# Kernel optimization log

Hardware: AMD Instinct MI355X
Metric: run time of the kernel (lower is better)

## Reference

```python
import jax, jax.numpy as jnp
import numpy as np

S, B, V, D, H, G = 60, 256, 50000, 300, 512, 15  # seq, batch, vocab, embed/proj, hidden, grid
DM, DOUT = 1024, 2
MLP_IN = G * G + 7  # 225 pooled + 7 extra features = 232


def setup_inputs() -> dict:
    key = jax.random.key(0)
    ks = jax.random.split(key, 16)
    n = lambda k, shp: (jax.random.normal(k, shp, jnp.float32) * 0.02)
    return {
        "embed_table": n(ks[0], (V, D)),
        "proj_W": n(ks[1], (D, D)),
        "proj_b": jnp.zeros((D,), jnp.float32),
        "bn_g": jnp.ones((D,), jnp.float32),
        "bn_b": jnp.zeros((D,), jnp.float32),
        "Wih": n(ks[2], (4 * H, D)),
        "Whh": n(ks[3], (4 * H, H)),
        "bih": jnp.zeros((4 * H,), jnp.float32),
        "bhh": jnp.zeros((4 * H,), jnp.float32),
        "W1": n(ks[4], (DM, MLP_IN)),
        "b1": jnp.zeros((DM,), jnp.float32),
        "g1": jnp.ones((DM,), jnp.float32),
        "be1": jnp.zeros((DM,), jnp.float32),
        "W2": n(ks[5], (DM, DM)),
        "b2": jnp.zeros((DM,), jnp.float32),
        "g2": jnp.ones((DM,), jnp.float32),
        "be2": jnp.zeros((DM,), jnp.float32),
        "W3": n(ks[6], (DOUT, DM)),
        "b3": jnp.zeros((DOUT,), jnp.float32),
        "extra_feats": jax.random.normal(ks[7], (B, 7), jnp.float32),
        "sentence1": jax.random.randint(ks[8], (S, B), 0, V, jnp.int32),
        "sentence2": jax.random.randint(ks[9], (S, B), 0, V, jnp.int32),
    }


def _bn(x, g, b, axes):
    mu = x.mean(axis=axes, keepdims=True)
    var = x.var(axis=axes, keepdims=True)
    return (x - mu) * jax.lax.rsqrt(var + 1e-5) * g + b


def reference(embed_table, proj_W, proj_b, bn_g, bn_b, Wih, Whh, bih, bhh,
              W1, b1, g1, be1, W2, b2, g2, be2, W3, b3,
              extra_feats, sentence1, sentence2):
    def encode(tokens):
        e = embed_table[tokens]                      # [S,B,D] gather
        e = e @ proj_W.T + proj_b                    # Bottle Linear over S*B rows
        e = _bn(e, bn_g, bn_b, (0, 1))               # Bottle BatchNorm over S*B rows

        def step(carry, x):
            h, c = carry
            z = x @ Wih.T + h @ Whh.T + (bih + bhh)  # [B,4H], gate order i,f,g,o
            i, f, g_, o = jnp.split(z, 4, axis=-1)
            c = jax.nn.sigmoid(f) * c + jax.nn.sigmoid(i) * jnp.tanh(g_)
            h = jax.nn.sigmoid(o) * jnp.tanh(c)
            return (h, c), h

        init = (jnp.zeros((B, H), e.dtype), jnp.zeros((B, H), e.dtype))
        _, hs = jax.lax.scan(step, init, e)          # [S,B,H]
        return hs.transpose(1, 0, 2)                 # [B,S,H]

    h1 = encode(sentence1)
    h2 = encode(sentence2)

    # pairwise L2 distance matrix per batch element: [B,S,S]
    sq = (jnp.sum(h1 * h1, -1)[:, :, None]
          + jnp.sum(h2 * h2, -1)[:, None, :]
          - 2.0 * jnp.einsum('bid,bjd->bij', h1, h2))
    dist = jnp.sqrt(jnp.maximum(sq, 0.0) + 1e-12)

    # dynamic 15x15 min-pool (S divisible by G => kernel = S//G)
    k = S // G
    pooled = dist.reshape(B, G, k, G, k).min(axis=(2, 4)).reshape(B, G * G)

    x = jnp.concatenate([pooled, extra_feats], axis=1)  # [B,232]
    x = _bn(jax.nn.relu(x @ W1.T + b1), g1, be1, (0,))
    x = _bn(jax.nn.relu(x @ W2.T + b2), g2, be2, (0,))
    return jax.nn.log_softmax(x @ W3.T + b3, axis=-1)   # [B,2]
```

## Files before the change

kernel.cpp:

```cpp
#include <hip/hip_runtime.h>
#include <hip/hip_bf16.h>

#define S_LEN 60
#define BATCH 256
#define EMB   300
#define EMBP  320
#define HID   512
#define DMLP  1024
#define NROW  (2*S_LEN*BATCH)
#define RPS   (S_LEN*BATCH)

typedef __attribute__((ext_vector_type(8))) short short8v;
typedef __attribute__((ext_vector_type(4))) float f32x4;

static __device__ __forceinline__ float sigf(float x){
  return 1.0f/(1.0f+__expf(-x));
}
static __device__ __forceinline__ float tanh_fast(float x){
  x = fminf(fmaxf(x,-40.0f),40.0f);
  float a = __expf(2.0f*x);
  return (a-1.0f)/(a+1.0f);
}
static __device__ __forceinline__ unsigned short f2b(float v){
  __hip_bfloat16 h = __float2bfloat16(v);
  return *(unsigned short*)&h;
}
static __device__ __forceinline__ float b2f(unsigned short u){
  return __uint_as_float(((unsigned int)u)<<16);
}

__global__ __launch_bounds__(256) void k_conv_weights(
    const float* __restrict__ Wih, const float* __restrict__ Whh,
    const float* __restrict__ bih, const float* __restrict__ bhh,
    const float* __restrict__ projW,
    unsigned short* __restrict__ Wihb, unsigned short* __restrict__ Whhb,
    unsigned short* __restrict__ projWb, float* __restrict__ bsum)
{
  const int tid = blockIdx.x*256 + threadIdx.x;
  const int stride = gridDim.x*256;
  for (int i=tid; i<2048*EMBP; i+=stride){
    int n = i/EMBP, k = i - n*EMBP;
    Wihb[i] = f2b((k<EMB) ? Wih[(size_t)n*EMB + k] : 0.0f);
  }
  for (int i=tid; i<2048*HID; i+=stride) Whhb[i] = f2b(Whh[i]);
  for (int i=tid; i<EMBP*EMBP; i+=stride){
    int n = i/EMBP, k = i - n*EMBP;
    projWb[i] = f2b((n<EMB && k<EMB) ? projW[(size_t)n*EMB + k] : 0.0f);
  }
  for (int i=tid; i<2048; i+=stride) bsum[i] = bih[i]+bhh[i];
}

__global__ __launch_bounds__(512) void k_embed_mfma(
    const float* __restrict__ embed, const unsigned short* __restrict__ projWb,
    const float* __restrict__ projb, const int* __restrict__ s1,
    const int* __restrict__ s2, unsigned short* __restrict__ Pb)
{
  __shared__ __align__(16) unsigned short sA0[64*40];
  __shared__ __align__(16) unsigned short sA1[64*40];
  __shared__ __align__(16) unsigned short sW0[64*40];
  __shared__ __align__(16) unsigned short sW1[64*40];
  __shared__ int stok[64];
  const int m0 = blockIdx.x*64, n0 = blockIdx.y*64;
  const int tid = threadIdx.x;
  if (tid < 64){
    int r = m0 + tid;
    stok[tid] = (r < RPS) ? s1[r] : s2[r-RPS];
  }
  __syncthreads();
  const int lane = tid & 63, w = tid>>6;
  const int wr = w>>2, wc = w&3;
  const bool isA = tid < 256;
  const int srow = (tid&255)>>2, sseg = tid&3;
  const float* Arow = embed + (size_t)stok[srow]*EMB;
  const unsigned short* Wrow = projWb + (size_t)(n0+srow)*EMBP;

  const int ldst = srow*40 + sseg*8;
  const int aoff0 = (wr*32 + (lane&15))*40 + (lane>>4)*8;
  const int aoff1 = aoff0 + 16*40;
  const int woff  = (wc*16 + (lane&15))*40 + (lane>>4)*8;

  f32x4 acc0 = {0.f,0.f,0.f,0.f}, acc1 = {0.f,0.f,0.f,0.f};

  auto loadA = [&](int kk)->uint4 {
    int kb = kk*32 + sseg*8;
    unsigned short t8[8];
    if (kb+7 < EMB){
      float4 f0 = *(const float4*)(Arow + kb);
      float4 f1 = *(const float4*)(Arow + kb + 4);
      t8[0]=f2b(f0.x); t8[1]=f2b(f0.y); t8[2]=f2b(f0.z); t8[3]=f2b(f0.w);
      t8[4]=f2b(f1.x); t8[5]=f2b(f1.y); t8[6]=f2b(f1.z); t8[7]=f2b(f1.w);
    } else {
      #pragma unroll
      for (int jq=0; jq<8; jq++){
        int k = kb+jq;
        t8[jq] = f2b((k<EMB) ? Arow[k] : 0.0f);
      }
    }
    uint4 o;
    o.x = (unsigned)t8[0] | ((unsigned)t8[1]<<16);
    o.y = (unsigned)t8[2] | ((unsigned)t8[3]<<16);
    o.z = (unsigned)t8[4] | ((unsigned)t8[5]<<16);
    o.w = (unsigned)t8[6] | ((unsigned)t8[7]<<16);
    return o;
  };

  if (isA) *(uint4*)(sA0 + ldst) = loadA(0);
  else     *(uint4*)(sW0 + ldst) = *(const uint4*)(Wrow + sseg*8);
  __syncthreads();

  for (int kk=0; kk<10; kk++){
    uint4 nv;
    if (kk < 9){
      if (isA) nv = loadA(kk+1);
      else     nv = *(const uint4*)(Wrow + (kk+1)*32 + sseg*8);
    }
    const unsigned short* A = (kk&1) ? sA1 : sA0;
    const unsigned short* W = (kk&1) ? sW1 : sW0;
    short8v af0 = *(const short8v*)(A + aoff0);
    short8v af1 = *(const short8v*)(A + aoff1);
    short8v wf  = *(const short8v*)(W + woff);
    acc0 = __builtin_amdgcn_mfma_f32_16x16x32_bf16(af0, wf, acc0, 0,0,0);
    acc1 = __builtin_amdgcn_mfma_f32_16x16x32_bf16(af1, wf, acc1, 0,0,0);
    if (kk < 9){
      unsigned short* dst = ((kk&1) ? (isA?sA0:sW0) : (isA?sA1:sW1)) + ldst;
      *(uint4*)dst = nv;
    }
    __syncthreads();
  }

  const int cc = wc*16 + (lane&15);
  const int n = n0 + cc;
  const float bias = (n < EMB) ? projb[n] : 0.0f;
  const bool valid = (n < EMB);
  #pragma unroll
  for (int v=0; v<4; v++){
    int r0 = wr*32 + (lane>>4)*4 + v;
    Pb[(size_t)(m0+r0)*EMBP + n]    = f2b(valid ? acc0[v]+bias : 0.0f);
    Pb[(size_t)(m0+r0+16)*EMBP + n] = f2b(valid ? acc1[v]+bias : 0.0f);
  }
}

__global__ __launch_bounds__(320) void k_bn_partial(const unsigned short* __restrict__ Pb,
    float* __restrict__ ps, float* __restrict__ psq)
{
  const int rb = blockIdx.x, sent = blockIdx.y, t = threadIdx.x;
  if (t >= EMB) return;
  const unsigned short* base = Pb + ((size_t)sent*RPS + (size_t)rb*256)*EMBP;
  float s=0.0f, q=0.0f;
  for (int r=0;r<256;r++){
    float v = b2f(base[(size_t)r*EMBP + t]);
    s += v; q = fmaf(v,v,q);
  }
  ps [(size_t)(sent*60+rb)*EMB + t] = s;
  psq[(size_t)(sent*60+rb)*EMB + t] = q;
}

__global__ __launch_bounds__(320) void k_bn_final(const float* __restrict__ ps,
    const float* __restrict__ psq, const float* __restrict__ g,
    const float* __restrict__ b, float* __restrict__ scale, float* __restrict__ shift)
{
  const int sent = blockIdx.x, t = threadIdx.x;
  if (t >= EMB) return;
  float s=0.0f, q=0.0f;
  for (int i=0;i<60;i++){
    s += ps [(size_t)(sent*60+i)*EMB + t];
    q += psq[(size_t)(sent*60+i)*EMB + t];
  }
  float mean = s * (1.0f/15360.0f);
  float var  = q * (1.0f/15360.0f) - mean*mean;
  float sc = g[t] * rsqrtf(var + 1e-5f);
  scale[sent*EMB+t] = sc;
  shift[sent*EMB+t] = b[t] - mean*sc;
}

__global__ __launch_bounds__(256) void k_bn_apply(unsigned short* __restrict__ Pb,
    const float* __restrict__ scale, const float* __restrict__ shift)
{
  const int r = blockIdx.x*8 + (threadIdx.x>>5);
  const int c0 = threadIdx.x & 31;
  const int sent = (r >= RPS) ? 1 : 0;
  unsigned short* row = Pb + (size_t)r*EMBP;
  for (int c=c0; c<EMB; c+=32){
    float v = b2f(row[c]);
    v = fmaf(v, scale[sent*EMB+c], shift[sent*EMB+c]);
    row[c] = f2b(v);
  }
}

__global__ __launch_bounds__(512) void k_lstm_step(
    const unsigned short* __restrict__ Pb,
    const unsigned short* __restrict__ Wihb,
    const unsigned short* __restrict__ Whhb,
    const float* __restrict__ bsum,
    const unsigned short* __restrict__ Hin,
    unsigned short* __restrict__ Hnext,
    float* __restrict__ cst,
    unsigned short* __restrict__ Hout,
    int tstep)
{
  __shared__ __align__(16) unsigned short smem[4*5120];
  float* zs = (float*)smem;

  const int tid = threadIdx.x;
  const int lane = tid & 63, w = tid >> 6;
  const int wr = w >> 2, wc = w & 3;
  const int j0 = (int)blockIdx.x * 16;
  const int m0 = (int)blockIdx.y * 64;
  const int sent = m0 >> 8;
  const int brow = m0 & 255;

  const int half = tid >> 8;
  const int rs = tid & 255;
  const int srow = rs >> 2, sseg = rs & 3;
  const int kb = half*32 + sseg*8;
  const int ldst = half*2560 + srow*40 + sseg*8;

  const unsigned short* pAx = Pb + ((size_t)((sent*S_LEN + tstep)*BATCH) + brow + srow)*EMBP + kb;
  const unsigned short* pAh = Hin + (size_t)(m0 + srow)*HID + kb;
  const int wn = (srow>>4)*HID + j0 + (srow&15);
  const unsigned short* pWx = Wihb + (size_t)wn*EMBP + kb;
  const unsigned short* pWh = Whhb + (size_t)wn*HID  + kb;

  auto loadA = [&](int c)->uint4 {
    return (c < 5) ? *(const uint4*)(pAx + c*64) : *(const uint4*)(pAh + (c-5)*64);
  };
  auto loadW = [&](int c)->uint4 {
    return (c < 5) ? *(const uint4*)(pWx + c*64) : *(const uint4*)(pWh + (c-5)*64);
  };

  const int aoffB = (wr*32 + (lane&15))*40 + (lane>>4)*8;
  const int woffB = (wc*16 + (lane&15))*40 + (lane>>4)*8;

  f32x4 acc0 = {0.f,0.f,0.f,0.f}, acc1 = {0.f,0.f,0.f,0.f};

  uint4 rA[3], rW[3];
  rA[0] = loadA(0); rW[0] = loadW(0);
  rA[1] = loadA(1); rW[1] = loadW(1);
  rA[2] = loadA(2); rW[2] = loadW(2);
  *(uint4*)(smem + ldst)         = rA[0];
  *(uint4*)(smem + 10240 + ldst) = rW[0];
  __syncthreads();

  #pragma unroll
  for (int kk = 0; kk < 13; kk++){
    if (kk + 3 < 13){
      rA[(kk+3)%3] = loadA(kk+3);
      rW[(kk+3)%3] = loadW(kk+3);
    }
    const unsigned short* A = smem + (kk&1)*5120;
    const unsigned short* W = smem + 10240 + (kk&1)*5120;
    #pragma unroll
    for (int h2 = 0; h2 < 2; h2++){
      const int bh = h2*2560;
      short8v wf = *(const short8v*)(W + bh + woffB);
      short8v a0 = *(const short8v*)(A + bh + aoffB);
      short8v a1 = *(const short8v*)(A + bh + aoffB + 16*40);
      acc0 = __builtin_amdgcn_mfma_f32_16x16x32_bf16(a0, wf, acc0, 0,0,0);
      acc1 = __builtin_amdgcn_mfma_f32_16x16x32_bf16(a1, wf, acc1, 0,0,0);
    }
    if (kk + 1 < 13){
      *(uint4*)(smem + ((kk+1)&1)*5120 + ldst)         = rA[(kk+1)%3];
      *(uint4*)(smem + 10240 + ((kk+1)&1)*5120 + ldst) = rW[(kk+1)%3];
    }
    __syncthreads();
  }

  #pragma unroll
  for (int v = 0; v < 4; v++){
    int r0 = wr*32 + (lane>>4)*4 + v;
    int cc = wc*16 + (lane&15);
    zs[r0*66 + cc]      = acc0[v];
    zs[(r0+16)*66 + cc] = acc1[v];
  }
  __syncthreads();

  const int row_e = tid >> 4, jj = tid & 15, j = j0 + jj;
  const float zb0 = bsum[0*HID+j], zb1 = bsum[1*HID+j];
  const float zb2 = bsum[2*HID+j], zb3 = bsum[3*HID+j];
  #pragma unroll
  for (int q = 0; q < 2; q++){
    int row = row_e + q*32;
    int r = m0 + row;
    float zi = zs[row*66 + jj]    + zb0;
    float zf = zs[row*66 + 16+jj] + zb1;
    float zg = zs[row*66 + 32+jj] + zb2;
    float zo = zs[row*66 + 48+jj] + zb3;
    size_t ci = (size_t)r*HID + j;
    float cn = fmaf(sigf(zf), cst[ci], sigf(zi)*tanh_fast(zg));
    cst[ci] = cn;
    float hn = sigf(zo)*tanh_fast(cn);
    unsigned short hb = f2b(hn);
    Hnext[ci] = hb;
    Hout[((size_t)((sent*S_LEN + tstep)*BATCH) + (r&255))*HID + j] = hb;
  }
}

#define SDU 258
__global__ __launch_bounds__(256) void k_dist_pool(
    const unsigned short* __restrict__ Hout, float* __restrict__ pooled)
{
  __shared__ unsigned int h1s[S_LEN*SDU];
  __shared__ unsigned int h2s[S_LEN*SDU];
  __shared__ float n1s[S_LEN], n2s[S_LEN];
  const int b = blockIdx.x, tid = threadIdx.x;
  const unsigned int* H = (const unsigned int*)Hout;
  for (int e=tid; e<S_LEN*256; e+=256){
    int row = e>>8, cu = e&255;
    h1s[row*SDU+cu] = H[((size_t)(0*S_LEN+row)*BATCH + b)*256 + cu];
    h2s[row*SDU+cu] = H[((size_t)(1*S_LEN+row)*BATCH + b)*256 + cu];
  }
  __syncthreads();
  if (tid < S_LEN){
    const unsigned int* rp = &h1s[tid*SDU];
    float q=0.0f;
    for (int cu=0;cu<256;cu++){
      unsigned int u = rp[cu];
      float lo = __uint_as_float(u<<16);
      float hi = __uint_as_float(u & 0xffff0000u);
      q = fmaf(lo,lo,q); q = fmaf(hi,hi,q);
    }
    n1s[tid] = q;
  } else if (tid >= 64 && tid < 64+S_LEN){
    const unsigned int* rp = &h2s[(tid-64)*SDU];
    float q=0.0f;
    for (int cu=0;cu<256;cu++){
      unsigned int u = rp[cu];
      float lo = __uint_as_float(u<<16);
      float hi = __uint_as_float(u & 0xffff0000u);
      q = fmaf(lo,lo,q); q = fmaf(hi,hi,q);
    }
    n2s[tid-64] = q;
  }
  __syncthreads();
  if (tid < 225){
    const int gi = tid/15, gj = tid%15;
    float acc[4][4];
    #pragma unroll
    for (int a=0;a<4;a++)
      #pragma unroll
      for (int c=0;c<4;c++) acc[a][c]=0.0f;
    const unsigned int* r1[4]; const unsigned int* r2[4];
    #pragma unroll
    for (int a=0;a<4;a++){ r1[a]=&h1s[(gi*4+a)*SDU]; r2[a]=&h2s[(gj*4+a)*SDU]; }
    for (int cu=0;cu<256;cu++){
      float lo1[4],hi1[4],lo2[4],hi2[4];
      #pragma unroll
      for (int a=0;a<4;a++){
        unsigned int u = r1[a][cu];
        lo1[a]=__uint_as_float(u<<16); hi1[a]=__uint_as_float(u&0xffff0000u);
      }
      #pragma unroll
      for (int c=0;c<4;c++){
        unsigned int u = r2[c][cu];
        lo2[c]=__uint_as_float(u<<16); hi2[c]=__uint_as_float(u&0xffff0000u);
      }
      #pragma unroll
      for (int a=0;a<4;a++)
        #pragma unroll
        for (int c=0;c<4;c++)
          acc[a][c] = fmaf(lo1[a],lo2[c], fmaf(hi1[a],hi2[c], acc[a][c]));
    }
    float mn = 3.4e38f;
    #pragma unroll
    for (int a=0;a<4;a++)
      #pragma unroll
      for (int c=0;c<4;c++){
        float sq = n1s[gi*4+a] + n2s[gj*4+c] - 2.0f*acc[a][c];
        mn = fminf(mn, sqrtf(fmaxf(sq,0.0f)+1e-12f));
      }
    pooled[(size_t)b*225 + tid] = mn;
  }
}

__global__ __launch_bounds__(256) void k_mlp1(const float* __restrict__ pooled,
    const float* __restrict__ extra, const float* __restrict__ W1,
    const float* __restrict__ b1, float* __restrict__ y1)
{
  __shared__ __align__(16) float xs[232];
  const int b = blockIdx.x, tid = threadIdx.x;
  if (tid < 225) xs[tid] = pooled[(size_t)b*225 + tid];
  else if (tid < 232) xs[tid] = extra[(size_t)b*7 + (tid-225)];
  __syncthreads();
  #pragma unroll
  for (int q=0;q<4;q++){
    int n = tid + q*256;
    float acc = b1[n];
    const float4* wr = (const float4*)(W1 + (size_t)n*232);
    const float4* xr = (const float4*)xs;
    for (int k4=0;k4<58;k4++){
      float4 w = wr[k4]; float4 x = xr[k4];
      acc = fmaf(w.x,x.x, fmaf(w.y,x.y, fmaf(w.z,x.z, fmaf(w.w,x.w, acc))));
    }
    y1[(size_t)b*DMLP + n] = fmaxf(acc, 0.0f);
  }
}

__global__ __launch_bounds__(256) void k_mlp_bn2(const float* __restrict__ y,
    const float* __restrict__ g, const float* __restrict__ be,
    float* __restrict__ scale, float* __restrict__ shift)
{
  __shared__ float sred[256], qred[256];
  const int c0 = blockIdx.x*64;
  const int ch = threadIdx.x & 63, grp = threadIdx.x >> 6;
  const int n = c0 + ch;
  float s=0.0f, q=0.0f;
  for (int b=grp*64; b<grp*64+64; b++){
    float v = y[(size_t)b*DMLP + n];
    s += v; q = fmaf(v,v,q);
  }
  sred[threadIdx.x]=s; qred[threadIdx.x]=q;
  __syncthreads();
  if (grp==0){
    s = sred[ch] + sred[64+ch] + sred[128+ch] + sred[192+ch];
    q = qred[ch] + qred[64+ch] + qred[128+ch] + qred[192+ch];
    float mean = s * (1.0f/256.0f);
    float var  = q * (1.0f/256.0f) - mean*mean;
    float sc = g[n] * rsqrtf(var + 1e-5f);
    scale[n] = sc;
    shift[n] = be[n] - mean*sc;
  }
}

__global__ __launch_bounds__(256) void k_mlp2_gemm(
    const float* __restrict__ y1, const float* __restrict__ scale1,
    const float* __restrict__ shift1, const float* __restrict__ W2,
    float* __restrict__ y2part)
{
  __shared__ float As[64][33];
  __shared__ float Bs[64][33];
  const int n0 = blockIdx.x*64, m0 = blockIdx.y*64;
  const int kbase = blockIdx.z*256;
  const int tid = threadIdx.x;
  const int tx = tid & 15, ty = tid >> 4;
  float acc[4][4];
  #pragma unroll
  for (int a=0;a<4;a++)
    #pragma unroll
    for (int b=0;b<4;b++) acc[a][b]=0.0f;

  for (int k0=0; k0<256; k0+=32){
    #pragma unroll
    for (int i=0;i<8;i++){
      int e = tid + i*256;
      int rl = e>>5, kl = e&31;
      int kk = kbase + k0 + kl;
      As[rl][kl] = fmaf(y1[(size_t)(m0+rl)*DMLP + kk], scale1[kk], shift1[kk]);
      Bs[rl][kl] = W2[(size_t)(n0+rl)*DMLP + kk];
    }
    __syncthreads();
    #pragma unroll
    for (int kk=0;kk<32;kk++){
      float a[4], w[4];
      #pragma unroll
      for (int rl=0;rl<4;rl++) a[rl] = As[ty*4+rl][kk];
      #pragma unroll
      for (int cj=0;cj<4;cj++) w[cj] = Bs[cj*16+tx][kk];
      #pragma unroll
      for (int rl=0;rl<4;rl++)
        #pragma unroll
        for (int cj=0;cj<4;cj++) acc[rl][cj] = fmaf(a[rl], w[cj], acc[rl][cj]);
    }
    __syncthreads();
  }
  float* dst = y2part + ((size_t)blockIdx.z*BATCH)*DMLP;
  #pragma unroll
  for (int rl=0;rl<4;rl++){
    int r = m0 + ty*4 + rl;
    #pragma unroll
    for (int cj=0;cj<4;cj++){
      int n = n0 + cj*16 + tx;
      dst[(size_t)r*DMLP + n] = acc[rl][cj];
    }
  }
}

__global__ __launch_bounds__(256) void k_mlp2_fin(
    const float* __restrict__ y2part, const float* __restrict__ b2,
    float* __restrict__ y2)
{
  const int b = blockIdx.x;
  const int n = threadIdx.x*4;
  float4 p0 = *(const float4*)(y2part + ((size_t)(0*BATCH + b))*DMLP + n);
  float4 p1 = *(const float4*)(y2part + ((size_t)(1*BATCH + b))*DMLP + n);
  float4 p2 = *(const float4*)(y2part + ((size_t)(2*BATCH + b))*DMLP + n);
  float4 p3 = *(const float4*)(y2part + ((size_t)(3*BATCH + b))*DMLP + n);
  float4 bb = *(const float4*)(b2 + n);
  float4 o;
  o.x = fmaxf(p0.x+p1.x+p2.x+p3.x+bb.x, 0.0f);
  o.y = fmaxf(p0.y+p1.y+p2.y+p3.y+bb.y, 0.0f);
  o.z = fmaxf(p0.z+p1.z+p2.z+p3.z+bb.z, 0.0f);
  o.w = fmaxf(p0.w+p1.w+p2.w+p3.w+bb.w, 0.0f);
  *(float4*)(y2 + (size_t)b*DMLP + n) = o;
}

__global__ __launch_bounds__(256) void k_mlp3(const float* __restrict__ y2,
    const float* __restrict__ scale2, const float* __restrict__ shift2,
    const float* __restrict__ W3, const float* __restrict__ b3,
    float* __restrict__ out)
{
  __shared__ float r0[256], r1[256];
  const int b = blockIdx.x, tid = threadIdx.x;
  float p0=0.0f, p1=0.0f;
  #pragma unroll
  for (int q=0;q<4;q++){
    int k = tid + q*256;
    float x = fmaf(y2[(size_t)b*DMLP + k], scale2[k], shift2[k]);
    p0 = fmaf(x, W3[k], p0);
    p1 = fmaf(x, W3[DMLP+k], p1);
  }
  r0[tid]=p0; r1[tid]=p1;
  __syncthreads();
  for (int s=128; s>0; s>>=1){
    if (tid<s){ r0[tid]+=r0[tid+s]; r1[tid]+=r1[tid+s]; }
    __syncthreads();
  }
  if (tid==0){
    float l0 = r0[0]+b3[0], l1 = r1[0]+b3[1];
    float m = fmaxf(l0,l1);
    float lse = m + logf(__expf(l0-m)+__expf(l1-m));
    out[b*2+0] = l0-lse;
    out[b*2+1] = l1-lse;
  }
}

extern "C" void kernel_launch(void* const* d_in, const int* in_sizes, int n_in,
                              void* d_out, int out_size, void* d_ws, size_t ws_size,
                              hipStream_t stream)
{
  (void)in_sizes; (void)n_in; (void)out_size; (void)ws_size;
  const float* embed = (const float*)d_in[0];
  const float* projW = (const float*)d_in[1];
  const float* projb = (const float*)d_in[2];
  const float* bn_g  = (const float*)d_in[3];
  const float* bn_b  = (const float*)d_in[4];
  const float* Wih   = (const float*)d_in[5];
  const float* Whh   = (const float*)d_in[6];
  const float* bih   = (const float*)d_in[7];
  const float* bhh   = (const float*)d_in[8];
  const float* W1    = (const float*)d_in[9];
  const float* b1    = (const float*)d_in[10];
  const float* g1    = (const float*)d_in[11];
  const float* be1   = (const float*)d_in[12];
  const float* W2    = (const float*)d_in[13];
  const float* b2    = (const float*)d_in[14];
  const float* g2    = (const float*)d_in[15];
  const float* be2   = (const float*)d_in[16];
  const float* W3    = (const float*)d_in[17];
  const float* b3    = (const float*)d_in[18];
  const float* extra = (const float*)d_in[19];
  const int*   s1    = (const int*)d_in[20];
  const int*   s2    = (const int*)d_in[21];
  float* out = (float*)d_out;

  float* ws = (float*)d_ws;
  size_t off = 0;
  float* ps   = ws + off; off += (size_t)2*60*EMB;
  float* psq  = ws + off; off += (size_t)2*60*EMB;
  float* bnsc = ws + off; off += 2*EMB;
  float* bnsh = ws + off; off += 2*EMB;
  float* bsum = ws + off; off += 2048;
  unsigned short* Pb     = (unsigned short*)(ws + off); off += (size_t)NROW*EMBP/2;
  unsigned short* Wihb   = (unsigned short*)(ws + off); off += (size_t)2048*EMBP/2;
  unsigned short* Whhb   = (unsigned short*)(ws + off); off += (size_t)2048*HID/2;
  unsigned short* projWb = (unsigned short*)(ws + off); off += (size_t)EMBP*EMBP/2;
  float* cst = ws + off; off += (size_t)512*HID;
  unsigned short* Hb0 = (unsigned short*)(ws + off); off += (size_t)512*HID/2;
  unsigned short* Hb1 = (unsigned short*)(ws + off); off += (size_t)512*HID/2;
  unsigned short* Hout = (unsigned short*)(ws + off); off += (size_t)2*S_LEN*BATCH*HID/2;
  float* pooled = ws + off; off += (size_t)BATCH*225;
  float* y1     = ws + off; off += (size_t)BATCH*DMLP;
  float* y2     = ws + off; off += (size_t)BATCH*DMLP;
  float* y2part = ws + off; off += (size_t)4*BATCH*DMLP;
  float* sc1    = ws + off; off += DMLP;
  float* sh1    = ws + off; off += DMLP;
  float* sc2    = ws + off; off += DMLP;
  float* sh2    = ws + off; off += DMLP;

  hipMemsetAsync(cst, 0, (size_t)(512*HID)*sizeof(float) + (size_t)(512*HID)*sizeof(unsigned short), stream);

  k_conv_weights<<<512, 256, 0, stream>>>(Wih, Whh, bih, bhh, projW,
                                          Wihb, Whhb, projWb, bsum);
  k_embed_mfma<<<dim3(NROW/64, 5), 512, 0, stream>>>(embed, projWb, projb, s1, s2, Pb);
  k_bn_partial<<<dim3(60,2), 320, 0, stream>>>(Pb, ps, psq);
  k_bn_final<<<2, 320, 0, stream>>>(ps, psq, bn_g, bn_b, bnsc, bnsh);
  k_bn_apply<<<NROW/8, 256, 0, stream>>>(Pb, bnsc, bnsh);

  for (int t=0; t<S_LEN; t++){
    const unsigned short* hin = (t & 1) ? Hb1 : Hb0;
    unsigned short*      hnxt = (t & 1) ? Hb0 : Hb1;
    k_lstm_step<<<dim3(32,8), 512, 0, stream>>>(Pb, Wihb, Whhb, bsum,
                                                hin, hnxt, cst, Hout, t);
  }

  k_dist_pool<<<BATCH, 256, 0, stream>>>(Hout, pooled);
  k_mlp1<<<BATCH, 256, 0, stream>>>(pooled, extra, W1, b1, y1);
  k_mlp_bn2<<<16, 256, 0, stream>>>(y1, g1, be1, sc1, sh1);
  k_mlp2_gemm<<<dim3(16,4,4), 256, 0, stream>>>(y1, sc1, sh1, W2, y2part);
  k_mlp2_fin<<<BATCH, 256, 0, stream>>>(y2part, b2, y2);
  k_mlp_bn2<<<16, 256, 0, stream>>>(y2, g2, be2, sc2, sh2);
  k_mlp3<<<BATCH, 256, 0, stream>>>(y2, sc2, sh2, W3, b3, out);
}
```

Before: 879.0 us.

## Widen LSTM step K-tile to 128 and tile the first MLP layer as a GEMM

The per-timestep LSTM kernel now stages 128 K columns per shared-memory stage instead of 64. This halves the number of barrier-separated iterations (7 instead of 13) at the cost of twice the LDS footprint. Separately, the first MLP layer moves from one block per batch row, which re-read all of W1 for every row, to a 64x64 register-tiled SIMT GEMM over a 16x4 grid. That GEMM reuses W1 and activations through shared memory, but runs far fewer blocks. The LSTM loop dominates the runtime because it is launched 60 times, so the fewer syncs per step are the main intended saving.

```diff
diff --git a/kernel.cpp b/kernel.cpp
--- a/kernel.cpp
+++ b/kernel.cpp
@@ -198,7 +198,7 @@
     unsigned short* __restrict__ Hout,
     int tstep)
 {
-  __shared__ __align__(16) unsigned short smem[4*5120];
+  __shared__ __align__(16) unsigned short smem[40960];
   float* zs = (float*)smem;
 
   const int tid = threadIdx.x;
@@ -209,23 +209,27 @@
   const int sent = m0 >> 8;
   const int brow = m0 & 255;
 
-  const int half = tid >> 8;
+  const int s0 = tid >> 8;
   const int rs = tid & 255;
   const int srow = rs >> 2, sseg = rs & 3;
-  const int kb = half*32 + sseg*8;
-  const int ldst = half*2560 + srow*40 + sseg*8;
-
-  const unsigned short* pAx = Pb + ((size_t)((sent*S_LEN + tstep)*BATCH) + brow + srow)*EMBP + kb;
-  const unsigned short* pAh = Hin + (size_t)(m0 + srow)*HID + kb;
+  const int kb0 = s0*32 + sseg*8;
+  const int kb1 = kb0 + 64;
+  const int ld0 = s0*2560 + srow*40 + sseg*8;
+  const int ld1 = ld0 + 5120;
+
+  const unsigned short* ArowP = Pb + ((size_t)((sent*S_LEN + tstep)*BATCH) + brow + srow)*EMBP;
+  const unsigned short* ArowH = Hin + (size_t)(m0 + srow)*HID;
   const int wn = (srow>>4)*HID + j0 + (srow&15);
-  const unsigned short* pWx = Wihb + (size_t)wn*EMBP + kb;
-  const unsigned short* pWh = Whhb + (size_t)wn*HID  + kb;
-
-  auto loadA = [&](int c)->uint4 {
-    return (c < 5) ? *(const uint4*)(pAx + c*64) : *(const uint4*)(pAh + (c-5)*64);
+  const unsigned short* WrowX = Wihb + (size_t)wn*EMBP;
+  const unsigned short* WrowH = Whhb + (size_t)wn*HID;
+
+  auto loadAc = [&](int col)->uint4 {
+    return (col < EMBP) ? *(const uint4*)(ArowP + col)
+                        : *(const uint4*)(ArowH + col - EMBP);
   };
-  auto loadW = [&](int c)->uint4 {
-    return (c < 5) ? *(const uint4*)(pWx + c*64) : *(const uint4*)(pWh + (c-5)*64);
+  auto loadWc = [&](int col)->uint4 {
+    return (col < EMBP) ? *(const uint4*)(WrowX + col)
+                        : *(const uint4*)(WrowH + col - EMBP);
   };
 
   const int aoffB = (wr*32 + (lane&15))*40 + (lane>>4)*8;
@@ -233,34 +237,50 @@
 
   f32x4 acc0 = {0.f,0.f,0.f,0.f}, acc1 = {0.f,0.f,0.f,0.f};
 
-  uint4 rA[3], rW[3];
-  rA[0] = loadA(0); rW[0] = loadW(0);
-  rA[1] = loadA(1); rW[1] = loadW(1);
-  rA[2] = loadA(2); rW[2] = loadW(2);
-  *(uint4*)(smem + ldst)         = rA[0];
-  *(uint4*)(smem + 10240 + ldst) = rW[0];
-  __syncthreads();
-
-  #pragma unroll
-  for (int kk = 0; kk < 13; kk++){
-    if (kk + 3 < 13){
-      rA[(kk+3)%3] = loadA(kk+3);
-      rW[(kk+3)%3] = loadW(kk+3);
-    }
-    const unsigned short* A = smem + (kk&1)*5120;
-    const unsigned short* W = smem + 10240 + (kk&1)*5120;
-    #pragma unroll
-    for (int h2 = 0; h2 < 2; h2++){
-      const int bh = h2*2560;
-      short8v wf = *(const short8v*)(W + bh + woffB);
-      short8v a0 = *(const short8v*)(A + bh + aoffB);
-      short8v a1 = *(const short8v*)(A + bh + aoffB + 16*40);
-      acc0 = __builtin_amdgcn_mfma_f32_16x16x32_bf16(a0, wf, acc0, 0,0,0);
-      acc1 = __builtin_amdgcn_mfma_f32_16x16x32_bf16(a1, wf, acc1, 0,0,0);
-    }
-    if (kk + 1 < 13){
-      *(uint4*)(smem + ((kk+1)&1)*5120 + ldst)         = rA[(kk+1)%3];
-      *(uint4*)(smem + 10240 + ((kk+1)&1)*5120 + ldst) = rW[(kk+1)%3];
+  {
+    uint4 a0 = loadAc(kb0), a1 = loadAc(kb1);
+    uint4 w0 = loadWc(kb0), w1 = loadWc(kb1);
+    *(uint4*)(smem + ld0) = a0;
+    *(uint4*)(smem + ld1) = a1;
+    *(uint4*)(smem + 20480 + ld0) = w0;
+    *(uint4*)(smem + 20480 + ld1) = w1;
+  }
+  __syncthreads();
+
+  #pragma unroll
+  for (int kk = 0; kk < 7; kk++){
+    uint4 pA0, pA1, pW0, pW1;
+    if (kk < 6){
+      int cbase = (kk+1)*128;
+      pA0 = loadAc(cbase + kb0);
+      pW0 = loadWc(cbase + kb0);
+      if (kk+1 < 6){
+        pA1 = loadAc(cbase + kb1);
+        pW1 = loadWc(cbase + kb1);
+      }
+    }
+    const unsigned short* A = smem + (kk&1)*10240;
+    const unsigned short* W = smem + 20480 + (kk&1)*10240;
+    #pragma unroll
+    for (int s = 0; s < 4; s++){
+      if (!(kk == 6 && s >= 2)){
+        const int bh = s*2560;
+        short8v wf  = *(const short8v*)(W + bh + woffB);
+        short8v a0f = *(const short8v*)(A + bh + aoffB);
+        short8v a1f = *(const short8v*)(A + bh + aoffB + 16*40);
+        acc0 = __builtin_amdgcn_mfma_f32_16x16x32_bf16(a0f, wf, acc0, 0,0,0);
+        acc1 = __builtin_amdgcn_mfma_f32_16x16x32_bf16(a1f, wf, acc1, 0,0,0);
+      }
+    }
+    if (kk < 6){
+      unsigned short* dA = smem + ((kk+1)&1)*10240;
+      unsigned short* dW = smem + 20480 + ((kk+1)&1)*10240;
+      *(uint4*)(dA + ld0) = pA0;
+      *(uint4*)(dW + ld0) = pW0;
+      if (kk+1 < 6){
+        *(uint4*)(dA + ld1) = pA1;
+        *(uint4*)(dW + ld1) = pW1;
+      }
     }
     __syncthreads();
   }
@@ -372,26 +392,58 @@
   }
 }
 
-__global__ __launch_bounds__(256) void k_mlp1(const float* __restrict__ pooled,
-    const float* __restrict__ extra, const float* __restrict__ W1,
-    const float* __restrict__ b1, float* __restrict__ y1)
-{
-  __shared__ __align__(16) float xs[232];
-  const int b = blockIdx.x, tid = threadIdx.x;
-  if (tid < 225) xs[tid] = pooled[(size_t)b*225 + tid];
-  else if (tid < 232) xs[tid] = extra[(size_t)b*7 + (tid-225)];
-  __syncthreads();
-  #pragma unroll
-  for (int q=0;q<4;q++){
-    int n = tid + q*256;
-    float acc = b1[n];
-    const float4* wr = (const float4*)(W1 + (size_t)n*232);
-    const float4* xr = (const float4*)xs;
-    for (int k4=0;k4<58;k4++){
-      float4 w = wr[k4]; float4 x = xr[k4];
-      acc = fmaf(w.x,x.x, fmaf(w.y,x.y, fmaf(w.z,x.z, fmaf(w.w,x.w, acc))));
-    }
-    y1[(size_t)b*DMLP + n] = fmaxf(acc, 0.0f);
+__global__ __launch_bounds__(256) void k_mlp1_gemm(
+    const float* __restrict__ pooled, const float* __restrict__ extra,
+    const float* __restrict__ W1, const float* __restrict__ b1,
+    float* __restrict__ y1)
+{
+  __shared__ float As[64][33];
+  __shared__ float Bs[64][33];
+  const int n0 = blockIdx.x*64, m0 = blockIdx.y*64;
+  const int tid = threadIdx.x;
+  const int tx = tid & 15, ty = tid >> 4;
+  float acc[4][4];
+  #pragma unroll
+  for (int a=0;a<4;a++)
+    #pragma unroll
+    for (int b=0;b<4;b++) acc[a][b]=0.0f;
+
+  for (int k0=0; k0<256; k0+=32){
+    #pragma unroll
+    for (int i=0;i<8;i++){
+      int e = tid + i*256;
+      int rl = e>>5, kl = e&31;
+      int c = k0 + kl;
+      float av;
+      if (c < 225)      av = pooled[(size_t)(m0+rl)*225 + c];
+      else if (c < 232) av = extra[(size_t)(m0+rl)*7 + (c-225)];
+      else              av = 0.0f;
+      As[rl][kl] = av;
+      Bs[rl][kl] = (c < 232) ? W1[(size_t)(n0+rl)*232 + c] : 0.0f;
+    }
+    __syncthreads();
+    #pragma unroll
+    for (int kk=0;kk<32;kk++){
+      float a[4], wv[4];
+      #pragma unroll
+      for (int rl=0;rl<4;rl++) a[rl] = As[ty*4+rl][kk];
+      #pragma unroll
+      for (int cj=0;cj<4;cj++) wv[cj] = Bs[cj*16+tx][kk];
+      #pragma unroll
+      for (int rl=0;rl<4;rl++)
+        #pragma unroll
+        for (int cj=0;cj<4;cj++) acc[rl][cj] = fmaf(a[rl], wv[cj], acc[rl][cj]);
+    }
+    __syncthreads();
+  }
+  #pragma unroll
+  for (int rl=0;rl<4;rl++){
+    int r = m0 + ty*4 + rl;
+    #pragma unroll
+    for (int cj=0;cj<4;cj++){
+      int n = n0 + cj*16 + tx;
+      y1[(size_t)r*DMLP + n] = fmaxf(acc[rl][cj] + b1[n], 0.0f);
+    }
   }
 }
 
@@ -593,7 +645,7 @@
   }
 
   k_dist_pool<<<BATCH, 256, 0, stream>>>(Hout, pooled);
-  k_mlp1<<<BATCH, 256, 0, stream>>>(pooled, extra, W1, b1, y1);
+  k_mlp1_gemm<<<dim3(16,4), 256, 0, stream>>>(pooled, extra, W1, b1, y1);
   k_mlp_bn2<<<16, 256, 0, stream>>>(y1, g1, be1, sc1, sh1);
   k_mlp2_gemm<<<dim3(16,4,4), 256, 0, stream>>>(y1, sc1, sh1, W2, y2part);
   k_mlp2_fin<<<BATCH, 256, 0, stream>>>(y2part, b2, y2);
```

Result: slower. 914.2 us (+4.0%).

## Tile MLP1 as shared-memory GEMM and pipeline loads in both MLP GEMMs

Applied to the files above, without the earlier changes.

Replaces the per-batch-row MLP1 kernel, which streamed all of W1 once for every batch row, with a 64x64 tiled shared-memory GEMM so W1 tiles are reused across 64 batch rows. Both MLP1 and MLP2 GEMMs now use double-buffered shared memory plus a three-deep register prefetch of upcoming K chunks, overlapping global loads with FMA work. The MLP1 grid shrinks to 64 blocks, which lowers parallelism, and register use rises from the prefetch buffers. These kernels are a small part of a runtime dominated by the 60-step LSTM loop.

```diff
diff --git a/kernel.cpp b/kernel.cpp
--- a/kernel.cpp
+++ b/kernel.cpp
@@ -372,26 +372,81 @@
   }
 }
 
-__global__ __launch_bounds__(256) void k_mlp1(const float* __restrict__ pooled,
-    const float* __restrict__ extra, const float* __restrict__ W1,
-    const float* __restrict__ b1, float* __restrict__ y1)
-{
-  __shared__ __align__(16) float xs[232];
-  const int b = blockIdx.x, tid = threadIdx.x;
-  if (tid < 225) xs[tid] = pooled[(size_t)b*225 + tid];
-  else if (tid < 232) xs[tid] = extra[(size_t)b*7 + (tid-225)];
-  __syncthreads();
-  #pragma unroll
-  for (int q=0;q<4;q++){
-    int n = tid + q*256;
-    float acc = b1[n];
-    const float4* wr = (const float4*)(W1 + (size_t)n*232);
-    const float4* xr = (const float4*)xs;
-    for (int k4=0;k4<58;k4++){
-      float4 w = wr[k4]; float4 x = xr[k4];
-      acc = fmaf(w.x,x.x, fmaf(w.y,x.y, fmaf(w.z,x.z, fmaf(w.w,x.w, acc))));
-    }
-    y1[(size_t)b*DMLP + n] = fmaxf(acc, 0.0f);
+__global__ __launch_bounds__(256) void k_mlp1_gemm(
+    const float* __restrict__ pooled, const float* __restrict__ extra,
+    const float* __restrict__ W1, const float* __restrict__ b1,
+    float* __restrict__ y1)
+{
+  __shared__ float As[2][64][33];
+  __shared__ float Bs[2][64][33];
+  const int n0 = blockIdx.x*64, m0 = blockIdx.y*64;
+  const int tid = threadIdx.x;
+  const int tx = tid & 15, ty = tid >> 4;
+  const int kl = tid & 31, r0s = tid >> 5;
+  float acc[4][4];
+  #pragma unroll
+  for (int a=0;a<4;a++)
+    #pragma unroll
+    for (int b=0;b<4;b++) acc[a][b]=0.0f;
+  float rA[3][8], rB[3][8];
+
+  auto loadC = [&](int ck, float* a8, float* b8){
+    int c = ck*32 + kl;
+    #pragma unroll
+    for (int i=0;i<8;i++){
+      int rl = r0s + i*8;
+      float av;
+      if (c < 225)      av = pooled[(size_t)(m0+rl)*225 + c];
+      else if (c < 232) av = extra[(size_t)(m0+rl)*7 + (c-225)];
+      else              av = 0.0f;
+      a8[i] = av;
+      b8[i] = (c < 232) ? W1[(size_t)(n0+rl)*232 + c] : 0.0f;
+    }
+  };
+
+  loadC(0, rA[0], rB[0]);
+  loadC(1, rA[1], rB[1]);
+  loadC(2, rA[2], rB[2]);
+  #pragma unroll
+  for (int i=0;i<8;i++){
+    As[0][r0s+i*8][kl] = rA[0][i];
+    Bs[0][r0s+i*8][kl] = rB[0][i];
+  }
+  __syncthreads();
+
+  #pragma unroll
+  for (int ck=0; ck<8; ck++){
+    if (ck+3 < 8) loadC(ck+3, rA[(ck+3)%3], rB[(ck+3)%3]);
+    const int pb = ck & 1;
+    #pragma unroll
+    for (int ki=0;ki<32;ki++){
+      float a[4], wv[4];
+      #pragma unroll
+      for (int rl=0;rl<4;rl++) a[rl] = As[pb][ty*4+rl][ki];
+      #pragma unroll
+      for (int cj=0;cj<4;cj++) wv[cj] = Bs[pb][cj*16+tx][ki];
+      #pragma unroll
+      for (int rl=0;rl<4;rl++)
+        #pragma unroll
+        for (int cj=0;cj<4;cj++) acc[rl][cj] = fmaf(a[rl], wv[cj], acc[rl][cj]);
+    }
+    if (ck+1 < 8){
+      #pragma unroll
+      for (int i=0;i<8;i++){
+        As[pb^1][r0s+i*8][kl] = rA[(ck+1)%3][i];
+        Bs[pb^1][r0s+i*8][kl] = rB[(ck+1)%3][i];
+      }
+    }
+    __syncthreads();
+  }
+  #pragma unroll
+  for (int rl=0;rl<4;rl++){
+    int r = m0 + ty*4 + rl;
+    #pragma unroll
+    for (int cj=0;cj<4;cj++){
+      int n = n0 + cj*16 + tx;
+      y1[(size_t)r*DMLP + n] = fmaxf(acc[rl][cj] + b1[n], 0.0f);
+    }
   }
 }
 
@@ -426,39 +481,63 @@
     const float* __restrict__ shift1, const float* __restrict__ W2,
     float* __restrict__ y2part)
 {
-  __shared__ float As[64][33];
-  __shared__ float Bs[64][33];
+  __shared__ float As[2][64][33];
+  __shared__ float Bs[2][64][33];
   const int n0 = blockIdx.x*64, m0 = blockIdx.y*64;
   const int kbase = blockIdx.z*256;
   const int tid = threadIdx.x;
   const int tx = tid & 15, ty = tid >> 4;
+  const int kl = tid & 31, r0s = tid >> 5;
   float acc[4][4];
   #pragma unroll
   for (int a=0;a<4;a++)
     #pragma unroll
     for (int b=0;b<4;b++) acc[a][b]=0.0f;
-
-  for (int k0=0; k0<256; k0+=32){
+  float rA[3][8], rB[3][8];
+
+  auto loadC = [&](int ck, float* a8, float* b8){
+    int c = kbase + ck*32 + kl;
+    float sc = scale1[c], sh = shift1[c];
     #pragma unroll
     for (int i=0;i<8;i++){
-      int e = tid + i*256;
-      int rl = e>>5, kl = e&31;
-      int kk = kbase + k0 + kl;
-      As[rl][kl] = fmaf(y1[(size_t)(m0+rl)*DMLP + kk], scale1[kk], shift1[kk]);
-      Bs[rl][kl] = W2[(size_t)(n0+rl)*DMLP + kk];
-    }
-    __syncthreads();
-    #pragma unroll
-    for (int kk=0;kk<32;kk++){
-      float a[4], w[4];
-      #pragma unroll
-      for (int rl=0;rl<4;rl++) a[rl] = As[ty*4+rl][kk];
-      #pragma unroll
-      for (int cj=0;cj<4;cj++) w[cj] = Bs[cj*16+tx][kk];
+      int rl = r0s + i*8;
+      a8[i] = fmaf(y1[(size_t)(m0+rl)*DMLP + c], sc, sh);
+      b8[i] = W2[(size_t)(n0+rl)*DMLP + c];
+    }
+  };
+
+  loadC(0, rA[0], rB[0]);
+  loadC(1, rA[1], rB[1]);
+  loadC(2, rA[2], rB[2]);
+  #pragma unroll
+  for (int i=0;i<8;i++){
+    As[0][r0s+i*8][kl] = rA[0][i];
+    Bs[0][r0s+i*8][kl] = rB[0][i];
+  }
+  __syncthreads();
+
+  #pragma unroll
+  for (int ck=0; ck<8; ck++){
+    if (ck+3 < 8) loadC(ck+3, rA[(ck+3)%3], rB[(ck+3)%3]);
+    const int pb = ck & 1;
+    #pragma unroll
+    for (int ki=0;ki<32;ki++){
+      float a[4], wv[4];
+      #pragma unroll
+      for (int rl=0;rl<4;rl++) a[rl] = As[pb][ty*4+rl][ki];
+      #pragma unroll
+      for (int cj=0;cj<4;cj++) wv[cj] = Bs[pb][cj*16+tx][ki];
       #pragma unroll
       for (int rl=0;rl<4;rl++)
         #pragma unroll
-        for (int cj=0;cj<4;cj++) acc[rl][cj] = fmaf(a[rl], w[cj], acc[rl][cj]);
+        for (int cj=0;cj<4;cj++) acc[rl][cj] = fmaf(a[rl], wv[cj], acc[rl][cj]);
+    }
+    if (ck+1 < 8){
+      #pragma unroll
+      for (int i=0;i<8;i++){
+        As[pb^1][r0s+i*8][kl] = rA[(ck+1)%3][i];
+        Bs[pb^1][r0s+i*8][kl] = rB[(ck+1)%3][i];
+      }
     }
     __syncthreads();
   }
@@ -593,7 +672,7 @@
   }
 
   k_dist_pool<<<BATCH, 256, 0, stream>>>(Hout, pooled);
-  k_mlp1<<<BATCH, 256, 0, stream>>>(pooled, extra, W1, b1, y1);
+  k_mlp1_gemm<<<dim3(16,4), 256, 0, stream>>>(pooled, extra, W1, b1, y1);
   k_mlp_bn2<<<16, 256, 0, stream>>>(y1, g1, be1, sc1, sh1);
   k_mlp2_gemm<<<dim3(16,4,4), 256, 0, stream>>>(y1, sc1, sh1, W2, y2part);
   k_mlp2_fin<<<BATCH, 256, 0, stream>>>(y2part, b2, y2);
```

Measured after the change: 1.026 ms. +16.7%, slower.
